# Kernel tuning notes

Hardware: AMD Instinct MI355X
Metric: run time of the kernel (lower is better)

Reference implementation:

```python
import jax, jax.numpy as jnp
import numpy as np

H = 1024
NH = 16
HD = H // NH

def setup_inputs() -> dict:
    key = jax.random.key(0)
    ks = jax.random.split(key, 10)
    s = 1.0 / np.sqrt(H)
    return {
        "hiddenStates": jax.random.normal(ks[0], (2, 2048, H), dtype=jnp.float32),
        "attentionMask": jnp.zeros((2, 1, 1, 2048), dtype=jnp.float32),
        "Wq": jax.random.uniform(ks[1], (H, H), jnp.float32, -s, s),
        "bq": jax.random.uniform(ks[2], (H,), jnp.float32, -s, s),
        "Wk": jax.random.uniform(ks[3], (H, H), jnp.float32, -s, s),
        "bk": jax.random.uniform(ks[4], (H,), jnp.float32, -s, s),
        "Wv": jax.random.uniform(ks[5], (H, H), jnp.float32, -s, s),
        "bv": jax.random.uniform(ks[6], (H,), jnp.float32, -s, s),
        "Wo": jax.random.uniform(ks[7], (H, H), jnp.float32, -s, s),
        "bo": jax.random.uniform(ks[8], (H,), jnp.float32, -s, s),
    }

def _split_heads(x):
    # [B,S,H] -> [B,NH,S,HD]
    b, s, _ = x.shape
    return x.reshape(b, s, NH, HD).transpose(0, 2, 1, 3)

def reference(hiddenStates, attentionMask, Wq, bq, Wk, bk, Wv, bv, Wo, bo):
    q = _split_heads(hiddenStates @ Wq.T + bq)
    k = _split_heads(hiddenStates @ Wk.T + bk)
    v = _split_heads(hiddenStates @ Wv.T + bv)
    scores = jnp.einsum('bhqd,bhkd->bhqk', q, k) / np.sqrt(HD)
    scores = scores + attentionMask
    probs = jax.nn.softmax(scores, axis=-1)  # dropout p=0 -> identity
    ctx = jnp.einsum('bhqk,bhkd->bhqd', probs, v)
    b, _, s, _ = ctx.shape
    ctx = ctx.transpose(0, 2, 1, 3).reshape(b, s, H)
    return ctx @ Wo.T + bo
```

## Files before the change

kernel.cpp:

```cpp
#include <hip/hip_runtime.h>


#define BB   2
#define SS   2048
#define HH   1024
#define NHH  16
#define HDD  64

#define LOG2E 1.4426950408889634f
#define C1    (0.125f * LOG2E)

typedef _Float16 h8 __attribute__((ext_vector_type(8)));
typedef float f32x4 __attribute__((ext_vector_type(4)));
typedef float f32x16 __attribute__((ext_vector_type(16)));
typedef unsigned short us8 __attribute__((ext_vector_type(8)));
typedef unsigned u32x2 __attribute__((ext_vector_type(2)));

static __device__ __forceinline__ unsigned short f2h(float f) {
  return __builtin_bit_cast(unsigned short, (_Float16)f);
}
static __device__ __forceinline__ float h2f(unsigned short h) {
  return (float)__builtin_bit_cast(_Float16, h);
}
static __device__ __forceinline__ f32x4 mfma16(us8 a, us8 b, f32x4 c) {
  return __builtin_amdgcn_mfma_f32_16x16x32_f16(
      __builtin_bit_cast(h8, a), __builtin_bit_cast(h8, b), c, 0, 0, 0);
}
static __device__ __forceinline__ f32x16 mfma32(us8 a, us8 b, f32x16 c) {
  return __builtin_amdgcn_mfma_f32_32x32x16_f16(
      __builtin_bit_cast(h8, a), __builtin_bit_cast(h8, b), c, 0, 0, 0);
}
static __device__ __forceinline__ void gload16(const void* g, void* l) {
  __builtin_amdgcn_global_load_lds(
      (const __attribute__((address_space(1))) unsigned int*)g,
      (__attribute__((address_space(3))) unsigned int*)l, 16, 0, 0);
}
static __device__ __forceinline__ float exp2fast(float x) {
  float r; asm("v_exp_f32 %0, %1" : "=v"(r) : "v"(x)); return r;
}
static __device__ __forceinline__ unsigned cvtpkh(float lo, float hi) {
  unsigned r;
  asm("v_cvt_pkrtz_f16_f32 %0, %1, %2" : "=v"(r) : "v"(lo), "v"(hi));
  return r;
}
static __device__ __forceinline__ void pl32swap(unsigned& a, unsigned& b) {
  u32x2 r = __builtin_amdgcn_permlane32_swap(a, b, false, false);
  a = r[0]; b = r[1];
}
static __device__ __forceinline__ int fragoff(int lg, int r) {
  return (((lg << 10) + (r << 3)) ^ (lg << 3));
}
static __device__ __forceinline__ us8 ldfrag(const void* base, int k, int bc) {
  const int byte =
      ((k >> 1) << 8) + (((((k & 1) << 7) | bc)) ^ (((k >> 1) & 7) << 4));
  return *(const us8*)((const char*)base + byte);
}

__global__ __launch_bounds__(256)
void pack_kernel(const float* __restrict__ X, const float* __restrict__ Wq,
                 const float* __restrict__ Wk, const float* __restrict__ Wv,
                 const float* __restrict__ Wo, const float* __restrict__ mask,
                 unsigned short* __restrict__ Xh,
                 unsigned short* __restrict__ Bh,
                 unsigned short* __restrict__ Oh,
                 float* __restrict__ maskl) {
  const int t = blockIdx.x;
  if (t == 2048) {
    const int i0 = threadIdx.x * 16;
#pragma unroll
    for (int j = 0; j < 4; ++j) {
      float4 v = *(const float4*)&mask[i0 + j * 4];
      v.x *= LOG2E; v.y *= LOG2E; v.z *= LOG2E; v.w *= LOG2E;
      *(float4*)&maskl[i0 + j * 4] = v;
    }
    return;
  }
  const float* src; unsigned short* dst;
  int smt, dmt, kt;
  if (t < 1024) { src = X; dst = Xh; smt = t >> 5; dmt = smt; kt = t & 31; }
  else {
    const int u = t - 1024, which = u >> 8, v = u & 255;
    smt = v >> 5; kt = v & 31;
    if (which == 0)      { src = Wq; dst = Bh; dmt = smt; }
    else if (which == 1) { src = Wk; dst = Bh; dmt = smt + 8; }
    else if (which == 2) { src = Wv; dst = Bh; dmt = smt + 16; }
    else                 { src = Wo; dst = Oh; dmt = smt; }
  }
  const size_t tb = ((size_t)(dmt * 32 + kt)) << 12;
#pragma unroll
  for (int it = 0; it < 2; ++it) {
    const int item = it * 256 + threadIdx.x;
    const int r = item >> 2, lg = item & 3;
    const float* sp = &src[(size_t)(smt * 128 + r) * HH + kt * 32 + lg * 8];
    const float4 a = *(const float4*)sp;
    const float4 b = *(const float4*)(sp + 4);
    const float vals[8] = {a.x, a.y, a.z, a.w, b.x, b.y, b.z, b.w};
    us8 h;
#pragma unroll
    for (int e = 0; e < 8; ++e) h[e] = f2h(vals[e]);
    *(us8*)&dst[tb + fragoff(lg, r)] = h;
  }
}

__global__ __launch_bounds__(256, 3)
void qkv_gemm_kernel(const unsigned short* __restrict__ Ah_,
                     const unsigned short* __restrict__ Bh_,
                     const float* __restrict__ bq, const float* __restrict__ bk,
                     const float* __restrict__ bv,
                     unsigned short* __restrict__ qb,
                     unsigned short* __restrict__ kb,
                     unsigned short* __restrict__ vt) {
  __shared__ __align__(16) unsigned short tiles[2][4096];
  const int tid = threadIdx.x, lane = tid & 63, wid = tid >> 6;
  const int l16 = lane & 15, lg = lane >> 4;
  const int wr = wid >> 1, wc = wid & 1;
  const int mt0 = blockIdx.y, nt0 = blockIdx.x;

  const unsigned short* gA = Ah_ + (((size_t)mt0 * 32) << 12);
  const unsigned short* gB = Bh_ + (((size_t)nt0 * 32) << 12);

  f32x4 acc[4][4] = {};
  for (int kt = 0; kt < 32; ++kt) {
    __syncthreads();
    const size_t ko = ((size_t)kt) << 12;
#pragma unroll
    for (int it = 0; it < 2; ++it) {
      const int c = it * 256 + tid;
      gload16(gA + ko + c * 8, (char*)&tiles[0][0] + c * 16);
      gload16(gB + ko + c * 8, (char*)&tiles[1][0] + c * 16);
    }
    __syncthreads();

    us8 a[4], b[4];
#pragma unroll
    for (int t = 0; t < 4; ++t) {
      a[t] = *(const us8*)&tiles[0][fragoff(lg, wr * 64 + t * 16 + l16)];
      b[t] = *(const us8*)&tiles[1][fragoff(lg, wc * 64 + t * 16 + l16)];
    }
#pragma unroll
    for (int mt = 0; mt < 4; ++mt)
#pragma unroll
      for (int nt = 0; nt < 4; ++nt)
        acc[mt][nt] = mfma16(a[mt], b[nt], acc[mt][nt]);
  }

  const int m0 = mt0 * 128, n0 = nt0 * 128;
#pragma unroll
  for (int nt = 0; nt < 4; ++nt) {
    const int col = n0 + wc * 64 + nt * 16 + l16;
    const int which = col >> 10, nn = col & 1023;
    const float bias = (which == 0) ? bq[nn] : ((which == 1) ? bk[nn] : bv[nn]);
    const int h = nn >> 6, d = nn & 63;
#pragma unroll
    for (int mt = 0; mt < 4; ++mt) {
      const int row0 = m0 + wr * 64 + mt * 16 + lg * 4;
      const int bi = row0 >> 11, si0 = row0 & 2047;
      const size_t head = (size_t)(bi * NHH + h);
      if (which == 2) {
        ushort4 vv;
#pragma unroll
        for (int reg = 0; reg < 4; ++reg)
          ((unsigned short*)&vv)[reg] = f2h(acc[mt][nt][reg] + bias);
        *(ushort4*)&vt[(head * HDD + d) * SS + si0] = vv;
      } else {
#pragma unroll
        for (int reg = 0; reg < 4; ++reg) {
          const unsigned short v16 = f2h(acc[mt][nt][reg] + bias);
          if (which == 0) qb[(head * SS + si0 + reg) * HDD + d] = v16;
          else            kb[(head * SS + si0 + reg) * HDD + d] = v16;
        }
      }
    }
  }
}

__global__ __launch_bounds__(512)
void attn_kernel(const unsigned short* __restrict__ qb,
                 const unsigned short* __restrict__ kbuf,
                 const unsigned short* __restrict__ vt,
                 const float* __restrict__ maskl,
                 unsigned short* __restrict__ Op,
                 float* __restrict__ Ls) {
  __shared__ __align__(16) unsigned short Klds[2][4096];
  __shared__ __align__(16) unsigned short Vlds[2][4096];
  __shared__ __align__(16) float Msk[2048];

  const int tid = threadIdx.x, lane = tid & 63, w = tid >> 6;
  const int q = lane & 31, hi = lane >> 5;
  const int bh = blockIdx.x;
  const int bi = bh >> 4, h = bh & 15;
  const int half = blockIdx.y >> 3;
  const int q0 = (blockIdx.y & 7) * 256 + w * 32;
  const int kbase = half * (SS / 2);
  const size_t bhS = (size_t)bh * SS;
  const int qrow = q0 + q;

  us8 qf[4];
#pragma unroll
  for (int ks = 0; ks < 4; ++ks)
    qf[ks] = *(const us8*)&qb[(bhS + qrow) * HDD + ks * 16 + hi * 8];

  f32x16 o0 = {}, o1 = {};
  float lrun = 0.0f;

#define STAGE(buf, kt_)                                                        \
  {                                                                            \
    const int key0_ = kbase + (kt_) * 64;                                      \
    const int row_ = tid >> 4;                       \
    const int ss_ = (tid & 15) ^ (row_ & 7);                                   \
    const int kd_ = 2 * row_ + (ss_ >> 3);                                     \
    const int el_ = (ss_ & 7) * 8;                                             \
    gload16(&kbuf[(bhS + key0_ + kd_) * HDD + el_],                            \
            (char*)&Klds[buf][0] + tid * 16);                                  \
    gload16(&vt[((size_t)bh * HDD + kd_) * SS + key0_ + el_],                  \
            (char*)&Vlds[buf][0] + tid * 16);                                  \
  }

  gload16(&maskl[bi * SS + tid * 4], (char*)&Msk[0] + tid * 16);
  STAGE(0, 0)
  __syncthreads();

  for (int kt = 0; kt < 16; ++kt) {
    const int buf = kt & 1;
    if (kt + 1 < 16) STAGE(buf ^ 1, kt + 1)
    const int ko = kbase + kt * 64;

    f32x16 s0 = {}, s1 = {};
    __builtin_amdgcn_s_setprio(1);
#pragma unroll
    for (int ks = 0; ks < 4; ++ks) {
      const int bc = ks * 32 + hi * 16;
      const us8 kf0 = ldfrag(&Klds[buf][0], q, bc);
      const us8 kf1 = ldfrag(&Klds[buf][0], 32 + q, bc);
      s0 = mfma32(kf0, qf[ks], s0);
      s1 = mfma32(kf1, qf[ks], s1);
    }
    __builtin_amdgcn_s_setprio(0);

#pragma unroll
    for (int g = 0; g < 4; ++g) {
      const float4 m0v = *(const float4*)&Msk[ko + g * 8 + hi * 4];
      const float4 m1v = *(const float4*)&Msk[ko + 32 + g * 8 + hi * 4];
      const float mm0[4] = {m0v.x, m0v.y, m0v.z, m0v.w};
      const float mm1[4] = {m1v.x, m1v.y, m1v.z, m1v.w};
#pragma unroll
      for (int j = 0; j < 4; ++j) {
        const int reg = g * 4 + j;
        s0[reg] = exp2fast(s0[reg] * C1 + mm0[j]);
        s1[reg] = exp2fast(s1[reg] * C1 + mm1[j]);
      }
    }
    float pa = 0.0f, pb_ = 0.0f, pc = 0.0f, pd = 0.0f;
#pragma unroll
    for (int g = 0; g < 4; ++g) {
      pa += s0[g * 4];     pb_ += s0[g * 4 + 1];
      pc += s0[g * 4 + 2]; pd += s0[g * 4 + 3];
      pa += s1[g * 4];     pb_ += s1[g * 4 + 1];
      pc += s1[g * 4 + 2]; pd += s1[g * 4 + 3];
    }
    float ps = (pa + pb_) + (pc + pd);
    ps += __shfl_xor(ps, 32);
    lrun += ps;

    us8 pb[4];
    {
      unsigned C[8];
#pragma unroll
      for (int j = 0; j < 8; ++j) C[j] = cvtpkh(s0[2 * j], s0[2 * j + 1]);
      pl32swap(C[0], C[2]); pl32swap(C[1], C[3]);
      pl32swap(C[4], C[6]); pl32swap(C[5], C[7]);
      union { unsigned wd[4]; us8 v; } u0, u1;
      u0.wd[0] = C[0]; u0.wd[1] = C[1]; u0.wd[2] = C[2]; u0.wd[3] = C[3];
      u1.wd[0] = C[4]; u1.wd[1] = C[5]; u1.wd[2] = C[6]; u1.wd[3] = C[7];
      pb[0] = u0.v; pb[1] = u1.v;
#pragma unroll
      for (int j = 0; j < 8; ++j) C[j] = cvtpkh(s1[2 * j], s1[2 * j + 1]);
      pl32swap(C[0], C[2]); pl32swap(C[1], C[3]);
      pl32swap(C[4], C[6]); pl32swap(C[5], C[7]);
      u0.wd[0] = C[0]; u0.wd[1] = C[1]; u0.wd[2] = C[2]; u0.wd[3] = C[3];
      u1.wd[0] = C[4]; u1.wd[1] = C[5]; u1.wd[2] = C[6]; u1.wd[3] = C[7];
      pb[2] = u0.v; pb[3] = u1.v;
    }

    __builtin_amdgcn_s_setprio(1);
#pragma unroll
    for (int kslice = 0; kslice < 4; ++kslice) {
      const int bc = kslice * 32 + hi * 16;
      const us8 vf0 = ldfrag(&Vlds[buf][0], q, bc);
      const us8 vf1 = ldfrag(&Vlds[buf][0], 32 + q, bc);
      o0 = mfma32(vf0, pb[kslice], o0);
      o1 = mfma32(vf1, pb[kslice], o1);
    }
    __builtin_amdgcn_s_setprio(0);

    __syncthreads();
  }

  unsigned short* op = Op + (((size_t)half * 32 + bh) * SS + qrow) * HDD;
#pragma unroll
  for (int g = 0; g < 4; ++g) {
    ushort4 v0, v1;
#pragma unroll
    for (int j = 0; j < 4; ++j) {
      ((unsigned short*)&v0)[j] = f2h(o0[g * 4 + j]);
      ((unsigned short*)&v1)[j] = f2h(o1[g * 4 + j]);
    }
    *(ushort4*)&op[g * 8 + hi * 4]      = v0;
    *(ushort4*)&op[32 + g * 8 + hi * 4] = v1;
  }
  if (hi == 0)
    Ls[((size_t)half * 32 + bh) * SS + qrow] = lrun;
#undef STAGE
}

__global__ __launch_bounds__(256)
void combine_kernel(const unsigned short* __restrict__ Op,
                    const float* __restrict__ Ls,
                    unsigned short* __restrict__ Ch) {
  const int gid = blockIdx.x * 256 + threadIdx.x;
  const int row = gid >> 2, qtr = gid & 3;
  const int bh = row >> 11, s = row & 2047;
  const int bi = bh >> 4, h = bh & 15;

  const float tot = Ls[row] + Ls[(size_t)65536 + row];
  const float rinv = 1.0f / tot;

  const int d0 = qtr * 16;
  const us8* p0 = (const us8*)&Op[(size_t)row * HDD + d0];
  const us8* p1 = (const us8*)&Op[(size_t)65536 * HDD + (size_t)row * HDD + d0];
  const us8 a0 = p0[0], a1 = p0[1], b0 = p1[0], b1 = p1[1];

  const int mrow = bi * SS + s;
  const int mt = mrow >> 7, r = mrow & 127;
#pragma unroll
  for (int j4 = 0; j4 < 4; ++j4) {
    const int col = h * 64 + d0 + j4 * 4;
    const int kt2 = col >> 5, lg2 = (col >> 3) & 3, e0 = col & 7;
    const size_t off = (((size_t)(mt * 32 + kt2)) << 12) + fragoff(lg2, r) + e0;
    ushort4 hv;
#pragma unroll
    for (int j = 0; j < 4; ++j) {
      const int k = j4 * 4 + j;
      const float va = h2f(k < 8 ? a0[k] : a1[k - 8]);
      const float vb = h2f(k < 8 ? b0[k] : b1[k - 8]);
      ((unsigned short*)&hv)[j] = f2h((va + vb) * rinv);
    }
    *(ushort4*)&Ch[off] = hv;
  }
}

__global__ __launch_bounds__(256, 3)
void out_gemm_kernel(const unsigned short* __restrict__ Ah_,
                     const unsigned short* __restrict__ Bh_,
                     const float* __restrict__ bo, float* __restrict__ out) {
  __shared__ __align__(16) unsigned short tiles[2][4096];
  const int tid = threadIdx.x, lane = tid & 63, wid = tid >> 6;
  const int l16 = lane & 15, lg = lane >> 4;
  const int wr = wid >> 1, wc = wid & 1;
  const int mt0 = blockIdx.y, nt0 = blockIdx.x;

  const unsigned short* gA = Ah_ + (((size_t)mt0 * 32) << 12);
  const unsigned short* gB = Bh_ + (((size_t)nt0 * 32) << 12);

  f32x4 acc[4][4] = {};
  for (int kt = 0; kt < 32; ++kt) {
    __syncthreads();
    const size_t ko = ((size_t)kt) << 12;
#pragma unroll
    for (int it = 0; it < 2; ++it) {
      const int c = it * 256 + tid;
      gload16(gA + ko + c * 8, (char*)&tiles[0][0] + c * 16);
      gload16(gB + ko + c * 8, (char*)&tiles[1][0] + c * 16);
    }
    __syncthreads();

    us8 a[4], b[4];
#pragma unroll
    for (int t = 0; t < 4; ++t) {
      a[t] = *(const us8*)&tiles[0][fragoff(lg, wr * 64 + t * 16 + l16)];
      b[t] = *(const us8*)&tiles[1][fragoff(lg, wc * 64 + t * 16 + l16)];
    }
#pragma unroll
    for (int mt = 0; mt < 4; ++mt)
#pragma unroll
      for (int nt = 0; nt < 4; ++nt)
        acc[mt][nt] = mfma16(a[mt], b[nt], acc[mt][nt]);
  }

  const int m0 = mt0 * 128, n0 = nt0 * 128;
#pragma unroll
  for (int nt = 0; nt < 4; ++nt) {
    const int col = n0 + wc * 64 + nt * 16 + l16;
    const float bias = bo[col];
#pragma unroll
    for (int mt = 0; mt < 4; ++mt)
#pragma unroll
      for (int reg = 0; reg < 4; ++reg) {
        const int row = m0 + wr * 64 + mt * 16 + lg * 4 + reg;
        out[(size_t)row * HH + col] = acc[mt][nt][reg] + bias;
      }
  }
}

extern "C" void kernel_launch(void* const* d_in, const int* in_sizes, int n_in,
                              void* d_out, int out_size, void* d_ws, size_t ws_size,
                              hipStream_t stream) {
  const float* X    = (const float*)d_in[0];
  const float* mask = (const float*)d_in[1];
  const float* Wq   = (const float*)d_in[2];
  const float* bq   = (const float*)d_in[3];
  const float* Wk   = (const float*)d_in[4];
  const float* bk   = (const float*)d_in[5];
  const float* Wv   = (const float*)d_in[6];
  const float* bv   = (const float*)d_in[7];
  const float* Wo   = (const float*)d_in[8];
  const float* bo   = (const float*)d_in[9];
  float* out = (float*)d_out;

  unsigned char* w = (unsigned char*)d_ws;
  const size_t MB = 1024 * 1024;
  unsigned short* Xh = (unsigned short*)(w);
  unsigned short* Bh = (unsigned short*)(w + 8 * MB);
  unsigned short* Oh = (unsigned short*)(w + 14 * MB);
  unsigned short* qb = (unsigned short*)(w + 16 * MB);
  unsigned short* kb = (unsigned short*)(w + 24 * MB);
  unsigned short* vt = (unsigned short*)(w + 32 * MB);
  unsigned short* Op = (unsigned short*)(w + 40 * MB);
  float*          Ls = (float*)(w + 56 * MB);
  float*       maskl = (float*)(w + 57 * MB);
  unsigned short* Ch = Xh;

  pack_kernel<<<2049, 256, 0, stream>>>(X, Wq, Wk, Wv, Wo, mask,
                                        Xh, Bh, Oh, maskl);
  qkv_gemm_kernel<<<dim3(24, 32), 256, 0, stream>>>(Xh, Bh, bq, bk, bv,
                                                    qb, kb, vt);
  attn_kernel<<<dim3(32, 16), 512, 0, stream>>>(qb, kb, vt, maskl, Op, Ls);
  combine_kernel<<<1024, 256, 0, stream>>>(Op, Ls, Ch);
  out_gemm_kernel<<<dim3(8, 32), 256, 0, stream>>>(Ch, Oh, bo, out);
}
```

Measured before the change: 198.6 us.

## Split attention keys four ways, double-buffer GEMM tiles, precompute LDS fragment offsets

```diff
diff --git a/kernel.cpp b/kernel.cpp
--- a/kernel.cpp
+++ b/kernel.cpp
@@ -50,10 +50,9 @@
 static __device__ __forceinline__ int fragoff(int lg, int r) {
   return (((lg << 10) + (r << 3)) ^ (lg << 3));
 }
-static __device__ __forceinline__ us8 ldfrag(const void* base, int k, int bc) {
-  const int byte =
-      ((k >> 1) << 8) + (((((k & 1) << 7) | bc)) ^ (((k >> 1) & 7) << 4));
-  return *(const us8*)((const char*)base + byte);
+static __device__ __forceinline__ int fragoff0(int k, int hi) {
+  return ((k >> 1) << 8) +
+         (((((k & 1) << 7) | (hi << 4))) ^ (((k >> 1) & 7) << 4));
 }
 
 __global__ __launch_bounds__(256)
@@ -110,7 +109,7 @@
                      unsigned short* __restrict__ qb,
                      unsigned short* __restrict__ kb,
                      unsigned short* __restrict__ vt) {
-  __shared__ __align__(16) unsigned short tiles[2][4096];
+  __shared__ __align__(16) unsigned short tiles[2][2][4096];
   const int tid = threadIdx.x, lane = tid & 63, wid = tid >> 6;
   const int l16 = lane & 15, lg = lane >> 4;
   const int wr = wid >> 1, wc = wid & 1;
@@ -119,30 +118,38 @@
   const unsigned short* gA = Ah_ + (((size_t)mt0 * 32) << 12);
   const unsigned short* gB = Bh_ + (((size_t)nt0 * 32) << 12);
 
+#define GSTAGE(buf, kt_)                                                       \
+  {                                                                            \
+    const size_t ko_ = ((size_t)(kt_)) << 12;                                  \
+    _Pragma("unroll")                                                          \
+    for (int it_ = 0; it_ < 2; ++it_) {                                        \
+      const int c_ = it_ * 256 + tid;                                          \
+      gload16(gA + ko_ + c_ * 8, (char*)&tiles[buf][0][0] + c_ * 16);          \
+      gload16(gB + ko_ + c_ * 8, (char*)&tiles[buf][1][0] + c_ * 16);          \
+    }                                                                          \
+  }
+
   f32x4 acc[4][4] = {};
+  GSTAGE(0, 0)
+  __syncthreads();
   for (int kt = 0; kt < 32; ++kt) {
-    __syncthreads();
-    const size_t ko = ((size_t)kt) << 12;
-#pragma unroll
-    for (int it = 0; it < 2; ++it) {
-      const int c = it * 256 + tid;
-      gload16(gA + ko + c * 8, (char*)&tiles[0][0] + c * 16);
-      gload16(gB + ko + c * 8, (char*)&tiles[1][0] + c * 16);
-    }
-    __syncthreads();
+    const int buf = kt & 1;
+    if (kt + 1 < 32) GSTAGE(buf ^ 1, kt + 1)
 
     us8 a[4], b[4];
 #pragma unroll
     for (int t = 0; t < 4; ++t) {
-      a[t] = *(const us8*)&tiles[0][fragoff(lg, wr * 64 + t * 16 + l16)];
-      b[t] = *(const us8*)&tiles[1][fragoff(lg, wc * 64 + t * 16 + l16)];
+      a[t] = *(const us8*)&tiles[buf][0][fragoff(lg, wr * 64 + t * 16 + l16)];
+      b[t] = *(const us8*)&tiles[buf][1][fragoff(lg, wc * 64 + t * 16 + l16)];
     }
 #pragma unroll
     for (int mt = 0; mt < 4; ++mt)
 #pragma unroll
       for (int nt = 0; nt < 4; ++nt)
         acc[mt][nt] = mfma16(a[mt], b[nt], acc[mt][nt]);
-  }
+    __syncthreads();
+  }
+#undef GSTAGE
 
   const int m0 = mt0 * 128, n0 = nt0 * 128;
 #pragma unroll
@@ -174,24 +181,27 @@
   }
 }
 
-__global__ __launch_bounds__(512)
+__global__ __launch_bounds__(512, 8)
 void attn_kernel(const unsigned short* __restrict__ qb,
                  const unsigned short* __restrict__ kbuf,
                  const unsigned short* __restrict__ vt,
                  const float* __restrict__ maskl,
-                 unsigned short* __restrict__ Op,
+                 unsigned short* __restrict__ Op0,
+                 unsigned short* __restrict__ Op1,
+                 unsigned short* __restrict__ Op2,
+                 unsigned short* __restrict__ Op3,
                  float* __restrict__ Ls) {
   __shared__ __align__(16) unsigned short Klds[2][4096];
   __shared__ __align__(16) unsigned short Vlds[2][4096];
-  __shared__ __align__(16) float Msk[2048];
+  __shared__ __align__(16) float Msk[512];
 
   const int tid = threadIdx.x, lane = tid & 63, w = tid >> 6;
   const int q = lane & 31, hi = lane >> 5;
   const int bh = blockIdx.x;
   const int bi = bh >> 4, h = bh & 15;
-  const int half = blockIdx.y >> 3;
+  const int quarter = blockIdx.y >> 3;
   const int q0 = (blockIdx.y & 7) * 256 + w * 32;
-  const int kbase = half * (SS / 2);
+  const int kbase = quarter * 512;
   const size_t bhS = (size_t)bh * SS;
   const int qrow = q0 + q;
 
@@ -199,6 +209,9 @@
 #pragma unroll
   for (int ks = 0; ks < 4; ++ks)
     qf[ks] = *(const us8*)&qb[(bhS + qrow) * HDD + ks * 16 + hi * 8];
+
+  const int koff0 = fragoff0(q, hi);
+  const int koff1 = fragoff0(32 + q, hi);
 
   f32x16 o0 = {}, o1 = {};
   float lrun = 0.0f;
@@ -216,22 +229,23 @@
             (char*)&Vlds[buf][0] + tid * 16);                                  \
   }
 
-  gload16(&maskl[bi * SS + tid * 4], (char*)&Msk[0] + tid * 16);
+  if (w < 2)
+    gload16(&maskl[bi * SS + kbase + tid * 4], (char*)&Msk[0] + tid * 16);
   STAGE(0, 0)
   __syncthreads();
 
-  for (int kt = 0; kt < 16; ++kt) {
+  for (int kt = 0; kt < 8; ++kt) {
     const int buf = kt & 1;
-    if (kt + 1 < 16) STAGE(buf ^ 1, kt + 1)
-    const int ko = kbase + kt * 64;
+    if (kt + 1 < 8) STAGE(buf ^ 1, kt + 1)
+    const char* kb0 = (const char*)&Klds[0][0] + buf * 8192;
+    const char* vb0 = (const char*)&Vlds[0][0] + buf * 8192;
 
     f32x16 s0 = {}, s1 = {};
     __builtin_amdgcn_s_setprio(1);
 #pragma unroll
     for (int ks = 0; ks < 4; ++ks) {
-      const int bc = ks * 32 + hi * 16;
-      const us8 kf0 = ldfrag(&Klds[buf][0], q, bc);
-      const us8 kf1 = ldfrag(&Klds[buf][0], 32 + q, bc);
+      const us8 kf0 = *(const us8*)(kb0 + (koff0 ^ (ks << 5)));
+      const us8 kf1 = *(const us8*)(kb0 + (koff1 ^ (ks << 5)));
       s0 = mfma32(kf0, qf[ks], s0);
       s1 = mfma32(kf1, qf[ks], s1);
     }
@@ -239,8 +253,8 @@
 
 #pragma unroll
     for (int g = 0; g < 4; ++g) {
-      const float4 m0v = *(const float4*)&Msk[ko + g * 8 + hi * 4];
-      const float4 m1v = *(const float4*)&Msk[ko + 32 + g * 8 + hi * 4];
+      const float4 m0v = *(const float4*)&Msk[kt * 64 + g * 8 + hi * 4];
+      const float4 m1v = *(const float4*)&Msk[kt * 64 + 32 + g * 8 + hi * 4];
       const float mm0[4] = {m0v.x, m0v.y, m0v.z, m0v.w};
       const float mm1[4] = {m1v.x, m1v.y, m1v.z, m1v.w};
 #pragma unroll
@@ -284,19 +298,20 @@
 
     __builtin_amdgcn_s_setprio(1);
 #pragma unroll
-    for (int kslice = 0; kslice < 4; ++kslice) {
-      const int bc = kslice * 32 + hi * 16;
-      const us8 vf0 = ldfrag(&Vlds[buf][0], q, bc);
-      const us8 vf1 = ldfrag(&Vlds[buf][0], 32 + q, bc);
-      o0 = mfma32(vf0, pb[kslice], o0);
-      o1 = mfma32(vf1, pb[kslice], o1);
+    for (int ks = 0; ks < 4; ++ks) {
+      const us8 vf0 = *(const us8*)(vb0 + (koff0 ^ (ks << 5)));
+      const us8 vf1 = *(const us8*)(vb0 + (koff1 ^ (ks << 5)));
+      o0 = mfma32(vf0, pb[ks], o0);
+      o1 = mfma32(vf1, pb[ks], o1);
     }
     __builtin_amdgcn_s_setprio(0);
 
     __syncthreads();
   }
 
-  unsigned short* op = Op + (((size_t)half * 32 + bh) * SS + qrow) * HDD;
+  unsigned short* opq = (quarter == 0) ? Op0 : (quarter == 1) ? Op1
+                       : (quarter == 2) ? Op2 : Op3;
+  unsigned short* op = opq + (bhS + qrow) * HDD;
 #pragma unroll
   for (int g = 0; g < 4; ++g) {
     ushort4 v0, v1;
@@ -309,12 +324,15 @@
     *(ushort4*)&op[32 + g * 8 + hi * 4] = v1;
   }
   if (hi == 0)
-    Ls[((size_t)half * 32 + bh) * SS + qrow] = lrun;
+    Ls[((size_t)quarter * 32 + bh) * SS + qrow] = lrun;
 #undef STAGE
 }
 
 __global__ __launch_bounds__(256)
-void combine_kernel(const unsigned short* __restrict__ Op,
+void combine_kernel(const unsigned short* __restrict__ Op0,
+                    const unsigned short* __restrict__ Op1,
+                    const unsigned short* __restrict__ Op2,
+                    const unsigned short* __restrict__ Op3,
                     const float* __restrict__ Ls,
                     unsigned short* __restrict__ Ch) {
   const int gid = blockIdx.x * 256 + threadIdx.x;
@@ -322,13 +340,19 @@
   const int bh = row >> 11, s = row & 2047;
   const int bi = bh >> 4, h = bh & 15;
 
-  const float tot = Ls[row] + Ls[(size_t)65536 + row];
+  const float tot = (Ls[row] + Ls[65536 + row]) +
+                    (Ls[131072 + row] + Ls[196608 + row]);
   const float rinv = 1.0f / tot;
 
   const int d0 = qtr * 16;
-  const us8* p0 = (const us8*)&Op[(size_t)row * HDD + d0];
-  const us8* p1 = (const us8*)&Op[(size_t)65536 * HDD + (size_t)row * HDD + d0];
-  const us8 a0 = p0[0], a1 = p0[1], b0 = p1[0], b1 = p1[1];
+  const us8* p0 = (const us8*)&Op0[(size_t)row * HDD + d0];
+  const us8* p1 = (const us8*)&Op1[(size_t)row * HDD + d0];
+  const us8* p2 = (const us8*)&Op2[(size_t)row * HDD + d0];
+  const us8* p3 = (const us8*)&Op3[(size_t)row * HDD + d0];
+  const us8 a0 = p0[0], a1 = p0[1];
+  const us8 b0 = p1[0], b1 = p1[1];
+  const us8 c0 = p2[0], c1 = p2[1];
+  const us8 d0v = p3[0], d1 = p3[1];
 
   const int mrow = bi * SS + s;
   const int mt = mrow >> 7, r = mrow & 127;
@@ -343,7 +367,9 @@
       const int k = j4 * 4 + j;
       const float va = h2f(k < 8 ? a0[k] : a1[k - 8]);
       const float vb = h2f(k < 8 ? b0[k] : b1[k - 8]);
-      ((unsigned short*)&hv)[j] = f2h((va + vb) * rinv);
+      const float vc = h2f(k < 8 ? c0[k] : c1[k - 8]);
+      const float vd = h2f(k < 8 ? d0v[k] : d1[k - 8]);
+      ((unsigned short*)&hv)[j] = f2h(((va + vb) + (vc + vd)) * rinv);
     }
     *(ushort4*)&Ch[off] = hv;
   }
@@ -353,7 +379,7 @@
 void out_gemm_kernel(const unsigned short* __restrict__ Ah_,
                      const unsigned short* __restrict__ Bh_,
                      const float* __restrict__ bo, float* __restrict__ out) {
-  __shared__ __align__(16) unsigned short tiles[2][4096];
+  __shared__ __align__(16) unsigned short tiles[2][2][4096];
   const int tid = threadIdx.x, lane = tid & 63, wid = tid >> 6;
   const int l16 = lane & 15, lg = lane >> 4;
   const int wr = wid >> 1, wc = wid & 1;
@@ -362,30 +388,38 @@
   const unsigned short* gA = Ah_ + (((size_t)mt0 * 32) << 12);
   const unsigned short* gB = Bh_ + (((size_t)nt0 * 32) << 12);
 
+#define GSTAGE(buf, kt_)                                                       \
+  {                                                                            \
+    const size_t ko_ = ((size_t)(kt_)) << 12;                                  \
+    _Pragma("unroll")                                                          \
+    for (int it_ = 0; it_ < 2; ++it_) {                                        \
+      const int c_ = it_ * 256 + tid;                                          \
+      gload16(gA + ko_ + c_ * 8, (char*)&tiles[buf][0][0] + c_ * 16);          \
+      gload16(gB + ko_ + c_ * 8, (char*)&tiles[buf][1][0] + c_ * 16);          \
+    }                                                                          \
+  }
+
   f32x4 acc[4][4] = {};
+  GSTAGE(0, 0)
+  __syncthreads();
   for (int kt = 0; kt < 32; ++kt) {
-    __syncthreads();
-    const size_t ko = ((size_t)kt) << 12;
-#pragma unroll
-    for (int it = 0; it < 2; ++it) {
-      const int c = it * 256 + tid;
-      gload16(gA + ko + c * 8, (char*)&tiles[0][0] + c * 16);
-      gload16(gB + ko + c * 8, (char*)&tiles[1][0] + c * 16);
-    }
-    __syncthreads();
+    const int buf = kt & 1;
+    if (kt + 1 < 32) GSTAGE(buf ^ 1, kt + 1)
 
     us8 a[4], b[4];
 #pragma unroll
     for (int t = 0; t < 4; ++t) {
-      a[t] = *(const us8*)&tiles[0][fragoff(lg, wr * 64 + t * 16 + l16)];
-      b[t] = *(const us8*)&tiles[1][fragoff(lg, wc * 64 + t * 16 + l16)];
+      a[t] = *(const us8*)&tiles[buf][0][fragoff(lg, wr * 64 + t * 16 + l16)];
+      b[t] = *(const us8*)&tiles[buf][1][fragoff(lg, wc * 64 + t * 16 + l16)];
     }
 #pragma unroll
     for (int mt = 0; mt < 4; ++mt)
 #pragma unroll
       for (int nt = 0; nt < 4; ++nt)
         acc[mt][nt] = mfma16(a[mt], b[nt], acc[mt][nt]);
-  }
+    __syncthreads();
+  }
+#undef GSTAGE
 
   const int m0 = mt0 * 128, n0 = nt0 * 128;
 #pragma unroll
@@ -419,22 +453,26 @@
 
   unsigned char* w = (unsigned char*)d_ws;
   const size_t MB = 1024 * 1024;
-  unsigned short* Xh = (unsigned short*)(w);
-  unsigned short* Bh = (unsigned short*)(w + 8 * MB);
-  unsigned short* Oh = (unsigned short*)(w + 14 * MB);
-  unsigned short* qb = (unsigned short*)(w + 16 * MB);
-  unsigned short* kb = (unsigned short*)(w + 24 * MB);
-  unsigned short* vt = (unsigned short*)(w + 32 * MB);
-  unsigned short* Op = (unsigned short*)(w + 40 * MB);
-  float*          Ls = (float*)(w + 56 * MB);
-  float*       maskl = (float*)(w + 57 * MB);
-  unsigned short* Ch = Xh;
+  unsigned short* Xh  = (unsigned short*)(w);
+  unsigned short* Bh  = (unsigned short*)(w + 8 * MB);
+  unsigned short* qb  = (unsigned short*)(w + 16 * MB);
+  unsigned short* kb  = (unsigned short*)(w + 24 * MB);
+  unsigned short* vt  = (unsigned short*)(w + 32 * MB);
+  unsigned short* Op0 = (unsigned short*)(w + 40 * MB);
+  unsigned short* Op1 = (unsigned short*)(w + 48 * MB);
+  unsigned short* Op2 = Xh;
+  unsigned short* Op3 = Bh;
+  unsigned short* Oh  = (unsigned short*)(w + 56 * MB);
+  float*          Ls  = (float*)(w + 58 * MB);
+  float*       maskl  = (float*)(w + 59 * MB);
+  unsigned short* Ch  = kb;
 
   pack_kernel<<<2049, 256, 0, stream>>>(X, Wq, Wk, Wv, Wo, mask,
                                         Xh, Bh, Oh, maskl);
   qkv_gemm_kernel<<<dim3(24, 32), 256, 0, stream>>>(Xh, Bh, bq, bk, bv,
                                                     qb, kb, vt);
-  attn_kernel<<<dim3(32, 16), 512, 0, stream>>>(qb, kb, vt, maskl, Op, Ls);
-  combine_kernel<<<1024, 256, 0, stream>>>(Op, Ls, Ch);
+  attn_kernel<<<dim3(32, 32), 512, 0, stream>>>(qb, kb, vt, maskl,
+                                                Op0, Op1, Op2, Op3, Ls);
+  combine_kernel<<<1024, 256, 0, stream>>>(Op0, Op1, Op2, Op3, Ls, Ch);
   out_gemm_kernel<<<dim3(8, 32), 256, 0, stream>>>(Ch, Oh, bo, out);
 }
```

New measurement: 437.1 us. +120.1%, slower.
